# Kernel tuning notes

Measured on AMD Instinct MI355X. Metric: run time of the kernel, lower is better.

Reference implementation:

```python
import jax, jax.numpy as jnp
import numpy as np

N = 100000
IN_DIM = 256
HID = 64
HEADS = 2
OUT_DIM = 64
E = 1600000
NEG_SLOPE = 0.2


def gat_conv(x, edge_index, W, att_src, att_dst, bias):
    # PyG GATConv with heads=HEADS, concat=True, add_self_loops=True.
    # x: [N, IN_DIM]; edge_index: [2, E] (row0=src, row1=dst)
    loops = jnp.arange(N, dtype=edge_index.dtype)
    src = jnp.concatenate([edge_index[0], loops])  # [E+N]
    dst = jnp.concatenate([edge_index[1], loops])  # [E+N]
    h = (x @ W).reshape(N, HEADS, HID)             # [N, H, C]
    a_src = jnp.einsum('nhc,hc->nh', h, att_src)   # [N, H]
    a_dst = jnp.einsum('nhc,hc->nh', h, att_dst)   # [N, H]
    e = jax.nn.leaky_relu(a_src[src] + a_dst[dst], NEG_SLOPE)  # [E+N, H]
    # segment softmax over incoming edges of each dst node
    m = jax.ops.segment_max(e, dst, num_segments=N)            # [N, H]
    p = jnp.exp(e - m[dst])
    denom = jax.ops.segment_sum(p, dst, num_segments=N)        # [N, H]
    alpha = p / denom[dst]                                     # [E+N, H]
    msg = h[src] * alpha[:, :, None]                           # [E+N, H, C]
    out = jax.ops.segment_sum(msg, dst, num_segments=N)        # [N, H, C]
    return out.reshape(N, HEADS * HID) + bias


def setup_inputs() -> dict:
    key = jax.random.key(0)
    ks = jax.random.split(key, 12)
    s_in = 1.0 / np.sqrt(IN_DIM)
    s_h = 1.0 / np.sqrt(HID)
    s_fc = 1.0 / np.sqrt(HEADS * HID * 2)
    return {
        'x': jax.random.normal(ks[0], (N, IN_DIM), jnp.float32),
        'edge_index_connected': jax.random.randint(ks[1], (2, E), 0, N, jnp.int32),
        'edge_index_liked': jax.random.randint(ks[2], (2, E), 0, N, jnp.int32),
        'W1': jax.random.normal(ks[3], (IN_DIM, HEADS * HID), jnp.float32) * s_in,
        'att_src1': jax.random.normal(ks[4], (HEADS, HID), jnp.float32) * s_h,
        'att_dst1': jax.random.normal(ks[5], (HEADS, HID), jnp.float32) * s_h,
        'b1': jnp.zeros((HEADS * HID,), jnp.float32),
        'W2': jax.random.normal(ks[6], (IN_DIM, HEADS * HID), jnp.float32) * s_in,
        'att_src2': jax.random.normal(ks[7], (HEADS, HID), jnp.float32) * s_h,
        'att_dst2': jax.random.normal(ks[8], (HEADS, HID), jnp.float32) * s_h,
        'b2': jnp.zeros((HEADS * HID,), jnp.float32),
        'fc_W': jax.random.normal(ks[9], (HEADS * HID * 2, OUT_DIM), jnp.float32) * s_fc,
        'fc_b': jnp.zeros((OUT_DIM,), jnp.float32),
    }


def reference(x, edge_index_connected, edge_index_liked, W1, att_src1, att_dst1, b1,
              W2, att_src2, att_dst2, b2, fc_W, fc_b):
    xc = jax.nn.relu(gat_conv(x, edge_index_connected, W1, att_src1, att_dst1, b1))
    xl = jax.nn.relu(gat_conv(x, edge_index_liked, W2, att_src2, att_dst2, b2))
    x_comb = jnp.concatenate([xc, xl], axis=1)  # [N, 4*HID]
    return x_comb @ fc_W + fc_b
```

## Files before the change

### kernel.cpp

```cpp
#include <hip/hip_runtime.h>
#include <hip/hip_fp16.h>
#include <math.h>

#define NN 100000
#define IN_DIM 256
#define HCH 128
#define OUT_DIM 64
#define EE 1600000
#define NEG_SLOPE 0.2f

#define NB 1024
#define NPB 98
#define CAP 2048

typedef _Float16 half8v __attribute__((ext_vector_type(8)));
typedef _Float16 half4v __attribute__((ext_vector_type(4)));
typedef _Float16 half2v __attribute__((ext_vector_type(2)));
typedef __fp16 fp16x2 __attribute__((ext_vector_type(2)));
typedef float float4v __attribute__((ext_vector_type(4)));
typedef unsigned int u32;

union H2U { u32 u; fp16x2 h; };

__device__ __forceinline__ float lrelu(float v) { return v > 0.f ? v : NEG_SLOPE * v; }

__global__ void convw_kernel(const float* __restrict__ W0, const float* __restrict__ W1,
                             const float* __restrict__ fcW,
                             _Float16* __restrict__ wt, _Float16* __restrict__ fcw2)
{
    int i = blockIdx.x * 256 + threadIdx.x;
    if (i < 2 * IN_DIM * HCH) {
        int l = i >> 15, rem = i & 32767;
        int c = rem >> 8, k = rem & 255;
        const float* W = l ? W1 : W0;
        wt[i] = (_Float16)W[(size_t)k * HCH + c];
        return;
    }
    int j = i - 2 * IN_DIM * HCH;
    if (j < 256 * OUT_DIM) {
        int c = j >> 8, k = j & 255;
        fcw2[j] = (_Float16)fcW[(size_t)k * OUT_DIM + c];
    }
}

__global__ __launch_bounds__(256, 3) void gemm_mfma(
    const float* __restrict__ x, const _Float16* __restrict__ wt,
    const float* __restrict__ attS0, const float* __restrict__ attD0,
    const float* __restrict__ attS1, const float* __restrict__ attD1,
    _Float16* __restrict__ h16, float* __restrict__ a_s, float* __restrict__ a_d, int n)
{
    __shared__ _Float16 smem[64 * 72 + 256 * 72];
    __shared__ float attv[4][128];
    _Float16 (*As)[72] = (_Float16(*)[72])smem;
    _Float16 (*Bs)[72] = (_Float16(*)[72])(smem + 64 * 72);
    const int tid = threadIdx.x;
    const int lane = tid & 63, wave = tid >> 6;
    const int wm = wave & 1, wn = wave >> 1;
    const int q = lane >> 4, r16 = lane & 15;
    const int row0 = blockIdx.x * 64;

    if (tid < 128) {
        attv[0][tid] = attS0[tid]; attv[1][tid] = attD0[tid];
        attv[2][tid] = attS1[tid]; attv[3][tid] = attD1[tid];
    }

    float4v acc[2][8];
#pragma unroll
    for (int i = 0; i < 2; ++i)
#pragma unroll
        for (int j = 0; j < 8; ++j) acc[i][j] = (float4v){0.f, 0.f, 0.f, 0.f};

    const int ar = tid >> 2, aq = tid & 3;
    const bool rok = (row0 + ar) < n;
    for (int kt = 0; kt < IN_DIM; kt += 64) {
        const float* xp = x + (size_t)(row0 + ar) * IN_DIM + kt + aq * 16;
#pragma unroll
        for (int i = 0; i < 4; ++i) {
            float4 v = rok ? *(const float4*)(xp + i * 4) : make_float4(0.f, 0.f, 0.f, 0.f);
            half4v hv = { (_Float16)v.x, (_Float16)v.y, (_Float16)v.z, (_Float16)v.w };
            *(half4v*)&As[ar][aq * 16 + i * 4] = hv;
        }
        const _Float16* wp = wt + (size_t)tid * IN_DIM + kt;
#pragma unroll
        for (int i = 0; i < 8; ++i)
            *(half8v*)&Bs[tid][i * 8] = *(const half8v*)(wp + i * 8);
        __syncthreads();
#pragma unroll
        for (int s = 0; s < 2; ++s) {
            half8v af[2], bf[8];
#pragma unroll
            for (int t = 0; t < 2; ++t)
                af[t] = *(half8v*)&As[wm * 32 + t * 16 + r16][s * 32 + q * 8];
#pragma unroll
            for (int t = 0; t < 8; ++t)
                bf[t] = *(half8v*)&Bs[wn * 128 + t * 16 + r16][s * 32 + q * 8];
#pragma unroll
            for (int mt = 0; mt < 2; ++mt)
#pragma unroll
                for (int nt = 0; nt < 8; ++nt)
                    acc[mt][nt] = __builtin_amdgcn_mfma_f32_16x16x32_f16(
                        af[mt], bf[nt], acc[mt][nt], 0, 0, 0);
        }
        __syncthreads();
    }
    _Float16 (*eb)[264] = (_Float16(*)[264])smem;
#pragma unroll
    for (int mt = 0; mt < 2; ++mt) {
        const int er = wm * 32 + mt * 16 + q * 4;
#pragma unroll
        for (int reg = 0; reg < 4; ++reg)
#pragma unroll
            for (int nt = 0; nt < 8; ++nt)
                eb[er + reg][wn * 128 + nt * 16 + r16] = (_Float16)acc[mt][nt][reg];
    }
    __syncthreads();
    const int r = tid >> 2, qq = tid & 3;
    const int grow = row0 + r;
    if (grow < n) {
        const int l2 = qq >> 1;
        const int hh = qq & 1;
        const float* avS = &attv[l2 * 2 + 0][hh * 64];
        const float* avD = &attv[l2 * 2 + 1][hh * 64];
        _Float16* hout = h16 + (size_t)l2 * NN * HCH + (size_t)grow * HCH + hh * 64;
        float ds = 0.f, dd = 0.f;
#pragma unroll
        for (int i = 0; i < 8; ++i) {
            half8v v = *(half8v*)&eb[r][qq * 64 + i * 8];
            *(half8v*)(hout + i * 8) = v;
#pragma unroll
            for (int j = 0; j < 8; ++j) {
                float f = (float)v[j];
                ds = fmaf(f, avS[i * 8 + j], ds);
                dd = fmaf(f, avD[i * 8 + j], dd);
            }
        }
        a_s[(size_t)l2 * 2 * NN + 2 * grow + hh] = ds;
        a_d[(size_t)l2 * 2 * NN + 2 * grow + hh] = dd;
    }
}

__global__ __launch_bounds__(1024) void bucket_kernel(const int* __restrict__ ei0,
                                                      const int* __restrict__ ei1,
                                                      int* __restrict__ gcursor,
                                                      int* __restrict__ bstore, int e)
{
    __shared__ int hist[NB];
    __shared__ int base[NB];
    const int lay = blockIdx.y;
    const int* src = lay ? ei1 : ei0;
    const int* dst = src + e;
    int* gcur = gcursor + lay * NB;
    int* bst = bstore + (size_t)lay * NB * CAP;

    const int tid = threadIdx.x;
    const int per = (e + gridDim.x - 1) / gridDim.x;
    const int e0 = blockIdx.x * per;
    const int e1 = min(e, e0 + per);
    for (int i = tid; i < NB; i += 1024) hist[i] = 0;
    __syncthreads();
    for (int i = e0 + tid; i < e1; i += 1024)
        atomicAdd(&hist[dst[i] / NPB], 1);
    __syncthreads();
    for (int b = tid; b < NB; b += 1024) {
        int c = hist[b];
        base[b] = c ? atomicAdd(&gcur[b], c) : 0;
        hist[b] = 0;
    }
    __syncthreads();
    for (int i = e0 + tid; i < e1; i += 1024) {
        int d = dst[i];
        int s = src[i];
        int b = d / NPB;
        int pos = base[b] + atomicAdd(&hist[b], 1);
        if (pos >= 0 && pos < CAP) bst[b * CAP + pos] = (s << 7) | (d - b * NPB);
    }
}

__global__ __launch_bounds__(256) void sort_kernel(
    const int* __restrict__ gcursor, int* __restrict__ bstore,
    int* __restrict__ gstart, int* __restrict__ gend, int n)
{
    __shared__ int raw[CAP];
    __shared__ int sorted[CAP];
    __shared__ int curs[128];
    __shared__ int scanbuf[128];
    const int lay = blockIdx.y;
    const int* gcur = gcursor + lay * NB;
    int* bst = bstore + (size_t)lay * NB * CAP;
    int* gs = gstart + (size_t)lay * NN;
    int* ge = gend + (size_t)lay * NN;

    const int tid = threadIdx.x;
    const int b = blockIdx.x;
    const int node0 = b * NPB;
    const int nnode = min(NPB, n - node0);
    if (nnode <= 0) return;
    int cnt = gcur[b];
    cnt = cnt < 0 ? 0 : (cnt > CAP ? CAP : cnt);

    for (int i = tid; i < cnt; i += 256) raw[i] = bst[b * CAP + i];
    if (tid < 128) curs[tid] = 0;
    __syncthreads();
    for (int i = tid; i < cnt; i += 256) atomicAdd(&curs[raw[i] & 127], 1);
    __syncthreads();
    if (tid < 128) scanbuf[tid] = curs[tid];
    __syncthreads();
    for (int off = 1; off < 128; off <<= 1) {
        int v = 0;
        if (tid < 128) { v = scanbuf[tid]; if (tid >= off) v += scanbuf[tid - off]; }
        __syncthreads();
        if (tid < 128) scanbuf[tid] = v;
        __syncthreads();
    }
    if (tid < 128) {
        int ex = tid ? scanbuf[tid - 1] : 0;
        curs[tid] = ex;
        if (tid < nnode) {
            gs[node0 + tid] = b * CAP + ex;
            ge[node0 + tid] = b * CAP + scanbuf[tid];
        }
    }
    __syncthreads();
    for (int i = tid; i < cnt; i += 256) {
        int item = raw[i];
        int pos = atomicAdd(&curs[item & 127], 1);
        if (pos >= 0 && pos < CAP) sorted[pos] = item >> 7;
    }
    __syncthreads();
    for (int i = tid; i < cnt; i += 256) bst[b * CAP + i] = sorted[i];
}

__global__ __launch_bounds__(256) void agg_kernel(
    const _Float16* __restrict__ h16, const float2* __restrict__ a_s,
    const float2* __restrict__ a_d, const int* __restrict__ gstart,
    const int* __restrict__ gend, const int* __restrict__ bstore,
    const float* __restrict__ bias0, const float* __restrict__ bias1,
    _Float16* __restrict__ xc16, int n)
{
    __shared__ __align__(16) uint2 sh[4][64];
    const int lay = blockIdx.y;
    const _Float16* hL = h16 + (size_t)lay * NN * HCH;
    const float2* asL = a_s + (size_t)lay * NN;
    const float2* adL = a_d + (size_t)lay * NN;
    const int* gsL = gstart + (size_t)lay * NN;
    const int* geL = gend + (size_t)lay * NN;
    const int* ssort = bstore + (size_t)lay * NB * CAP;
    const float* bias = lay ? bias1 : bias0;

    const int wid = threadIdx.x >> 6, lane = threadIdx.x & 63;
    const int wbase = (blockIdx.x * 4 + wid) * 4;
    const int cl = lane & 15;
    const int w2 = lane >> 4;
    const int hh = cl >> 3;
    const u32 psel = hh ? 0x07060302u : 0x05040100u;
    const fp16x2 one2 = { (__fp16)1.f, (__fp16)1.f };

    float bv[8];
#pragma unroll
    for (int j = 0; j < 8; ++j) bv[j] = bias[cl * 8 + j];

    for (int ni = 0; ni < 4; ++ni) {
        const int node = wbase + ni;
        const bool valid = node < n;
        const int nn = valid ? node : 0;
        int start = gsL[nn], end = geL[nn];
        start = start < 0 ? 0 : (start > NB * CAP ? NB * CAP : start);
        end = end < start ? start : (end > NB * CAP ? NB * CAP : end);
        const float2 ad = adL[nn];
        const float2 asn = asL[nn];

        float acc[8] = {0.f, 0.f, 0.f, 0.f, 0.f, 0.f, 0.f, 0.f};
        float den = 0.f;

        for (int base = start; base < end; base += 64) {
            const int j = base + lane;
            const int cnt = min(64, end - base);
            float p0 = 0.f, p1 = 0.f;
            int s = 0;
            if (j < end) {
                s = ssort[j];
                if ((unsigned)s >= (unsigned)n) s = 0;
                float2 a = asL[s];
                p0 = __expf(lrelu(a.x + ad.x));
                p1 = __expf(lrelu(a.y + ad.y));
            }
            H2U pk; pk.h = __builtin_amdgcn_cvt_pkrtz(p0, p1);
            sh[wid][lane] = make_uint2((u32)s, pk.u);
            __builtin_amdgcn_wave_barrier();
            const int cnt8 = (cnt + 7) & ~7;
            for (int t = 0; t < cnt8; t += 8) {
                const uint4 rec = *(const uint4*)&sh[wid][t + 2 * w2];
                H2U pph; pph.u = __builtin_amdgcn_perm(rec.w, rec.y, psel);
                const half8v hv0 = *(const half8v*)(hL + ((rec.x << 7) | (u32)(cl << 3)));
                const half8v hv1 = *(const half8v*)(hL + ((rec.z << 7) | (u32)(cl << 3)));
                const u32* ap = (const u32*)&hv0;
                const u32* bp = (const u32*)&hv1;
#pragma unroll
                for (int d2 = 0; d2 < 4; ++d2) {
                    H2U pe, po;
                    pe.u = __builtin_amdgcn_perm(bp[d2], ap[d2], 0x05040100u);
                    po.u = __builtin_amdgcn_perm(bp[d2], ap[d2], 0x07060302u);
                    acc[2 * d2]     = __builtin_amdgcn_fdot2(pe.h, pph.h, acc[2 * d2], false);
                    acc[2 * d2 + 1] = __builtin_amdgcn_fdot2(po.h, pph.h, acc[2 * d2 + 1], false);
                }
                den = __builtin_amdgcn_fdot2(pph.h, one2, den, false);
            }
            __builtin_amdgcn_wave_barrier();
        }
        const float ps0 = __expf(lrelu(asn.x + ad.x));
        const float ps1 = __expf(lrelu(asn.y + ad.y));
        if (w2 == 0) {
            const half8v hv = *(const half8v*)(hL + (((u32)nn << 7) | (u32)(cl << 3)));
            const float pl = hh ? ps1 : ps0;
#pragma unroll
            for (int j2 = 0; j2 < 8; ++j2)
                acc[j2] = fmaf(pl, (float)hv[j2], acc[j2]);
            den += pl;
        }
#pragma unroll
        for (int j2 = 0; j2 < 8; ++j2) {
            acc[j2] += __shfl_xor(acc[j2], 16, 64);
            acc[j2] += __shfl_xor(acc[j2], 32, 64);
        }
        den += __shfl_xor(den, 16, 64);
        den += __shfl_xor(den, 32, 64);
        if (valid && lane < 16) {
            const float inv = 1.f / den;
            half8v o;
#pragma unroll
            for (int j2 = 0; j2 < 8; ++j2)
                o[j2] = (_Float16)fmaxf(acc[j2] * inv + bv[j2], 0.f);
            *(half8v*)(xc16 + (size_t)node * 256 + lay * HCH + cl * 8) = o;
        }
    }
}

__global__ __launch_bounds__(256) void fc_mfma(const _Float16* __restrict__ xc16,
                                               const _Float16* __restrict__ fw2,
                                               const float* __restrict__ fcb,
                                               float* __restrict__ out, int n)
{
    __shared__ _Float16 axs[64][264];
    const int tid = threadIdx.x;
    const int lane = tid & 63, wave = tid >> 6;
    const int q = lane >> 4, r16 = lane & 15;
    const int row0 = blockIdx.x * 64;

#pragma unroll
    for (int i = 0; i < 8; ++i) {
        const int idx = i * 256 + tid;
        const int row = idx >> 5;
        const int kg = (idx & 31) * 8;
        half8v v = { 0, 0, 0, 0, 0, 0, 0, 0 };
        if (row0 + row < n)
            v = *(const half8v*)(xc16 + (size_t)(row0 + row) * 256 + kg);
        *(half8v*)&axs[row][kg] = v;
    }
    __syncthreads();

    float4v acc[4];
#pragma unroll
    for (int i = 0; i < 4; ++i) acc[i] = (float4v){0.f, 0.f, 0.f, 0.f};
#pragma unroll
    for (int s = 0; s < 8; ++s) {
        const half8v af = *(half8v*)&axs[wave * 16 + r16][s * 32 + q * 8];
#pragma unroll
        for (int nt = 0; nt < 4; ++nt) {
            const half8v bf =
                *(const half8v*)(fw2 + (size_t)(nt * 16 + r16) * 256 + s * 32 + q * 8);
            acc[nt] = __builtin_amdgcn_mfma_f32_16x16x32_f16(af, bf, acc[nt], 0, 0, 0);
        }
    }
#pragma unroll
    for (int nt = 0; nt < 4; ++nt) {
        const int col = nt * 16 + r16;
#pragma unroll
        for (int reg = 0; reg < 4; ++reg) {
            const int row = row0 + wave * 16 + q * 4 + reg;
            if (row < n)
                out[(size_t)row * OUT_DIM + col] = acc[nt][reg] + fcb[col];
        }
    }
}

extern "C" void kernel_launch(void* const* d_in, const int* in_sizes, int n_in,
                              void* d_out, int out_size, void* d_ws, size_t ws_size,
                              hipStream_t stream)
{
    const float* x = (const float*)d_in[0];
    const int* ei[2] = { (const int*)d_in[1], (const int*)d_in[2] };
    const float* W[2] = { (const float*)d_in[3], (const float*)d_in[7] };
    const float* attS[2] = { (const float*)d_in[4], (const float*)d_in[8] };
    const float* attD[2] = { (const float*)d_in[5], (const float*)d_in[9] };
    const float* bias[2] = { (const float*)d_in[6], (const float*)d_in[10] };
    const float* fcW = (const float*)d_in[11];
    const float* fcb = (const float*)d_in[12];
    float* out = (float*)d_out;

    char* p = (char*)d_ws;
    size_t need = 0;
    auto carve = [&](size_t bytes) {
        char* r = p;
        size_t b = (bytes + 255) & ~(size_t)255;
        p += b;
        need += b;
        return r;
    };
    _Float16* h16 = (_Float16*)carve((size_t)2 * NN * HCH * 2);
    _Float16* xc16 = (_Float16*)carve((size_t)NN * 256 * 2);
    _Float16* wt = (_Float16*)carve((size_t)2 * IN_DIM * HCH * 2);
    _Float16* fcw2 = (_Float16*)carve((size_t)256 * OUT_DIM * 2);
    float* a_s = (float*)carve((size_t)2 * NN * 8);
    float* a_d = (float*)carve((size_t)2 * NN * 8);
    int* gcursor = (int*)carve((size_t)2 * NB * 4);
    int* bstore = (int*)carve((size_t)2 * NB * CAP * 4);
    int* gstart = (int*)carve((size_t)2 * NN * 4);
    int* gend = (int*)carve((size_t)2 * NN * 4);
    if (need > ws_size) return;

    const int gemm_blocks = (NN + 63) / 64;
    const int agg_blocks = (NN + 15) / 16;
    const int conv_total = 2 * IN_DIM * HCH + 256 * OUT_DIM;

    convw_kernel<<<(conv_total + 255) / 256, 256, 0, stream>>>(W[0], W[1], fcW, wt, fcw2);

    gemm_mfma<<<gemm_blocks, 256, 0, stream>>>(x, wt, attS[0], attD[0], attS[1], attD[1],
                                               h16, a_s, a_d, NN);

    (void)hipMemsetAsync(gcursor, 0, (size_t)2 * NB * 4, stream);
    bucket_kernel<<<dim3(256, 2), 1024, 0, stream>>>(ei[0], ei[1], gcursor, bstore, EE);
    sort_kernel<<<dim3(NB, 2), 256, 0, stream>>>(gcursor, bstore, gstart, gend, NN);
    agg_kernel<<<dim3(agg_blocks, 2), 256, 0, stream>>>(
        h16, (const float2*)a_s, (const float2*)a_d,
        gstart, gend, bstore, bias[0], bias[1], xc16, NN);
    fc_mfma<<<gemm_blocks, 256, 0, stream>>>(xc16, fcw2, fcb, out, NN);
}
```

Before: 464.9 us.

## Merge launches: fuse weight conversion with bucketing, GEMM with sort, aggregation with FC

The six launches become three. Weight conversion and edge bucketing share one grid, and the dense GEMM and per-bucket counting sort are interleaved across one grid. Aggregation of both layers now runs in a single block per 16 nodes, with the FC MFMA applied straight from shared memory. This removes the xc16 intermediate write and read plus the launch gaps, but it means smaller bucket blocks (256 threads) and possibly lower occupancy from the larger shared footprint in the fused kernels.

Result: slower. 478.7 us (+3.0%).

```diff
diff --git a/kernel.cpp b/kernel.cpp
--- a/kernel.cpp
+++ b/kernel.cpp
@@ -13,9 +13,13 @@
 #define NPB 98
 #define CAP 2048
 
+#define GEMM_BLOCKS 1563
+#define CONV_BLOCKS 320
+#define BUCKET_PER_LAYER 512
+#define SORT_BLOCKS (2 * NB)
+
 typedef _Float16 half8v __attribute__((ext_vector_type(8)));
 typedef _Float16 half4v __attribute__((ext_vector_type(4)));
-typedef _Float16 half2v __attribute__((ext_vector_type(2)));
 typedef __fp16 fp16x2 __attribute__((ext_vector_type(2)));
 typedef float float4v __attribute__((ext_vector_type(4)));
 typedef unsigned int u32;
@@ -24,40 +28,142 @@
 
 __device__ __forceinline__ float lrelu(float v) { return v > 0.f ? v : NEG_SLOPE * v; }
 
-__global__ void convw_kernel(const float* __restrict__ W0, const float* __restrict__ W1,
-                             const float* __restrict__ fcW,
-                             _Float16* __restrict__ wt, _Float16* __restrict__ fcw2)
+__global__ __launch_bounds__(256, 8) void prep_kernel(
+    const float* __restrict__ W0, const float* __restrict__ W1,
+    const float* __restrict__ fcW,
+    _Float16* __restrict__ wt, _Float16* __restrict__ fcw2,
+    const int* __restrict__ ei0, const int* __restrict__ ei1,
+    int* __restrict__ gcursor, int* __restrict__ bstore)
 {
-    int i = blockIdx.x * 256 + threadIdx.x;
-    if (i < 2 * IN_DIM * HCH) {
-        int l = i >> 15, rem = i & 32767;
-        int c = rem >> 8, k = rem & 255;
-        const float* W = l ? W1 : W0;
-        wt[i] = (_Float16)W[(size_t)k * HCH + c];
+    __shared__ int hist[NB];
+    __shared__ int base[NB];
+    const int tid = threadIdx.x;
+
+    if (blockIdx.x < CONV_BLOCKS) {
+        int i = blockIdx.x * 256 + tid;
+        if (i < 2 * IN_DIM * HCH) {
+            int l = i >> 15, rem = i & 32767;
+            int c = rem >> 8, k = rem & 255;
+            const float* W = l ? W1 : W0;
+            wt[i] = (_Float16)W[(size_t)k * HCH + c];
+            return;
+        }
+        int j = i - 2 * IN_DIM * HCH;
+        if (j < 256 * OUT_DIM) {
+            int c = j >> 8, k = j & 255;
+            fcw2[j] = (_Float16)fcW[(size_t)k * OUT_DIM + c];
+        }
         return;
     }
-    int j = i - 2 * IN_DIM * HCH;
-    if (j < 256 * OUT_DIM) {
-        int c = j >> 8, k = j & 255;
-        fcw2[j] = (_Float16)fcW[(size_t)k * OUT_DIM + c];
+
+    const int bb = blockIdx.x - CONV_BLOCKS;
+    const int lay = bb >> 9;
+    const int idx = bb & 511;
+    const int* src = lay ? ei1 : ei0;
+    const int* dst = src + EE;
+    int* gcur = gcursor + lay * NB;
+    int* bst = bstore + (size_t)lay * NB * CAP;
+
+    const int per = (EE + BUCKET_PER_LAYER - 1) / BUCKET_PER_LAYER;
+    const int e0 = idx * per;
+    const int e1 = min(EE, e0 + per);
+    for (int i = tid; i < NB; i += 256) hist[i] = 0;
+    __syncthreads();
+    for (int i = e0 + tid; i < e1; i += 256)
+        atomicAdd(&hist[dst[i] / NPB], 1);
+    __syncthreads();
+    for (int b = tid; b < NB; b += 256) {
+        int c = hist[b];
+        base[b] = c ? atomicAdd(&gcur[b], c) : 0;
+        hist[b] = 0;
+    }
+    __syncthreads();
+    for (int i = e0 + tid; i < e1; i += 256) {
+        int d = dst[i];
+        int s = src[i];
+        int b = d / NPB;
+        int pos = base[b] + atomicAdd(&hist[b], 1);
+        if (pos >= 0 && pos < CAP) bst[b * CAP + pos] = (s << 7) | (d - b * NPB);
     }
 }
 
-__global__ __launch_bounds__(256, 3) void gemm_mfma(
+__global__ __launch_bounds__(256, 3) void mid_kernel(
     const float* __restrict__ x, const _Float16* __restrict__ wt,
     const float* __restrict__ attS0, const float* __restrict__ attD0,
     const float* __restrict__ attS1, const float* __restrict__ attD1,
-    _Float16* __restrict__ h16, float* __restrict__ a_s, float* __restrict__ a_d, int n)
+    _Float16* __restrict__ h16, float* __restrict__ a_s, float* __restrict__ a_d,
+    const int* __restrict__ gcursor, int* __restrict__ bstore,
+    int* __restrict__ gstart, int* __restrict__ gend, int n)
 {
-    __shared__ _Float16 smem[64 * 72 + 256 * 72];
+    __shared__ __align__(16) _Float16 smem[64 * 72 + 256 * 72];
     __shared__ float attv[4][128];
+    const int tid = threadIdx.x;
+
+    const long long TS = SORT_BLOCKS;
+    const long long TB = GEMM_BLOCKS + SORT_BLOCKS;
+    const int k = blockIdx.x;
+    const int slo = (int)(((long long)k * TS) / TB);
+    const int shi = (int)(((long long)(k + 1) * TS) / TB);
+
+    if (shi > slo) {
+        int* raw = (int*)smem;
+        int* sorted = raw + CAP;
+        int* curs = sorted + CAP;
+        int* scanbuf = curs + 128;
+        const int sb = slo;
+        const int lay = sb >> 10;
+        const int b = sb & (NB - 1);
+        const int* gcur = gcursor + lay * NB;
+        int* bst = bstore + (size_t)lay * NB * CAP;
+        int* gs = gstart + (size_t)lay * NN;
+        int* ge = gend + (size_t)lay * NN;
+
+        const int node0 = b * NPB;
+        const int nnode = min(NPB, n - node0);
+        if (nnode <= 0) return;
+        int cnt = gcur[b];
+        cnt = cnt < 0 ? 0 : (cnt > CAP ? CAP : cnt);
+
+        for (int i = tid; i < cnt; i += 256) raw[i] = bst[b * CAP + i];
+        if (tid < 128) curs[tid] = 0;
+        __syncthreads();
+        for (int i = tid; i < cnt; i += 256) atomicAdd(&curs[raw[i] & 127], 1);
+        __syncthreads();
+        if (tid < 128) scanbuf[tid] = curs[tid];
+        __syncthreads();
+        for (int off = 1; off < 128; off <<= 1) {
+            int v = 0;
+            if (tid < 128) { v = scanbuf[tid]; if (tid >= off) v += scanbuf[tid - off]; }
+            __syncthreads();
+            if (tid < 128) scanbuf[tid] = v;
+            __syncthreads();
+        }
+        if (tid < 128) {
+            int ex = tid ? scanbuf[tid - 1] : 0;
+            curs[tid] = ex;
+            if (tid < nnode) {
+                gs[node0 + tid] = b * CAP + ex;
+                ge[node0 + tid] = b * CAP + scanbuf[tid];
+            }
+        }
+        __syncthreads();
+        for (int i = tid; i < cnt; i += 256) {
+            int item = raw[i];
+            int pos = atomicAdd(&curs[item & 127], 1);
+            if (pos >= 0 && pos < CAP) sorted[pos] = item >> 7;
+        }
+        __syncthreads();
+        for (int i = tid; i < cnt; i += 256) bst[b * CAP + i] = sorted[i];
+        return;
+    }
+
     _Float16 (*As)[72] = (_Float16(*)[72])smem;
     _Float16 (*Bs)[72] = (_Float16(*)[72])(smem + 64 * 72);
-    const int tid = threadIdx.x;
+    const int gb = k - slo;
     const int lane = tid & 63, wave = tid >> 6;
     const int wm = wave & 1, wn = wave >> 1;
     const int q = lane >> 4, r16 = lane & 15;
-    const int row0 = blockIdx.x * 64;
+    const int row0 = gb * 64;
 
     if (tid < 128) {
         attv[0][tid] = attS0[tid]; attv[1][tid] = attD0[tid];
@@ -139,247 +245,132 @@
     }
 }
 
-__global__ __launch_bounds__(1024) void bucket_kernel(const int* __restrict__ ei0,
-                                                      const int* __restrict__ ei1,
-                                                      int* __restrict__ gcursor,
-                                                      int* __restrict__ bstore, int e)
-{
-    __shared__ int hist[NB];
-    __shared__ int base[NB];
-    const int lay = blockIdx.y;
-    const int* src = lay ? ei1 : ei0;
-    const int* dst = src + e;
-    int* gcur = gcursor + lay * NB;
-    int* bst = bstore + (size_t)lay * NB * CAP;
-
-    const int tid = threadIdx.x;
-    const int per = (e + gridDim.x - 1) / gridDim.x;
-    const int e0 = blockIdx.x * per;
-    const int e1 = min(e, e0 + per);
-    for (int i = tid; i < NB; i += 1024) hist[i] = 0;
-    __syncthreads();
-    for (int i = e0 + tid; i < e1; i += 1024)
-        atomicAdd(&hist[dst[i] / NPB], 1);
-    __syncthreads();
-    for (int b = tid; b < NB; b += 1024) {
-        int c = hist[b];
-        base[b] = c ? atomicAdd(&gcur[b], c) : 0;
-        hist[b] = 0;
-    }
-    __syncthreads();
-    for (int i = e0 + tid; i < e1; i += 1024) {
-        int d = dst[i];
-        int s = src[i];
-        int b = d / NPB;
-        int pos = base[b] + atomicAdd(&hist[b], 1);
-        if (pos >= 0 && pos < CAP) bst[b * CAP + pos] = (s << 7) | (d - b * NPB);
-    }
-}
-
-__global__ __launch_bounds__(256) void sort_kernel(
-    const int* __restrict__ gcursor, int* __restrict__ bstore,
-    int* __restrict__ gstart, int* __restrict__ gend, int n)
-{
-    __shared__ int raw[CAP];
-    __shared__ int sorted[CAP];
-    __shared__ int curs[128];
-    __shared__ int scanbuf[128];
-    const int lay = blockIdx.y;
-    const int* gcur = gcursor + lay * NB;
-    int* bst = bstore + (size_t)lay * NB * CAP;
-    int* gs = gstart + (size_t)lay * NN;
-    int* ge = gend + (size_t)lay * NN;
-
-    const int tid = threadIdx.x;
-    const int b = blockIdx.x;
-    const int node0 = b * NPB;
-    const int nnode = min(NPB, n - node0);
-    if (nnode <= 0) return;
-    int cnt = gcur[b];
-    cnt = cnt < 0 ? 0 : (cnt > CAP ? CAP : cnt);
-
-    for (int i = tid; i < cnt; i += 256) raw[i] = bst[b * CAP + i];
-    if (tid < 128) curs[tid] = 0;
-    __syncthreads();
-    for (int i = tid; i < cnt; i += 256) atomicAdd(&curs[raw[i] & 127], 1);
-    __syncthreads();
-    if (tid < 128) scanbuf[tid] = curs[tid];
-    __syncthreads();
-    for (int off = 1; off < 128; off <<= 1) {
-        int v = 0;
-        if (tid < 128) { v = scanbuf[tid]; if (tid >= off) v += scanbuf[tid - off]; }
-        __syncthreads();
-        if (tid < 128) scanbuf[tid] = v;
-        __syncthreads();
-    }
-    if (tid < 128) {
-        int ex = tid ? scanbuf[tid - 1] : 0;
-        curs[tid] = ex;
-        if (tid < nnode) {
-            gs[node0 + tid] = b * CAP + ex;
-            ge[node0 + tid] = b * CAP + scanbuf[tid];
-        }
-    }
-    __syncthreads();
-    for (int i = tid; i < cnt; i += 256) {
-        int item = raw[i];
-        int pos = atomicAdd(&curs[item & 127], 1);
-        if (pos >= 0 && pos < CAP) sorted[pos] = item >> 7;
-    }
-    __syncthreads();
-    for (int i = tid; i < cnt; i += 256) bst[b * CAP + i] = sorted[i];
-}
-
-__global__ __launch_bounds__(256) void agg_kernel(
+__global__ __launch_bounds__(256) void agg_fc(
     const _Float16* __restrict__ h16, const float2* __restrict__ a_s,
     const float2* __restrict__ a_d, const int* __restrict__ gstart,
     const int* __restrict__ gend, const int* __restrict__ bstore,
     const float* __restrict__ bias0, const float* __restrict__ bias1,
-    _Float16* __restrict__ xc16, int n)
+    const _Float16* __restrict__ fw2, const float* __restrict__ fcb,
+    float* __restrict__ out, int n)
 {
     __shared__ __align__(16) uint2 sh[4][64];
-    const int lay = blockIdx.y;
-    const _Float16* hL = h16 + (size_t)lay * NN * HCH;
-    const float2* asL = a_s + (size_t)lay * NN;
-    const float2* adL = a_d + (size_t)lay * NN;
-    const int* gsL = gstart + (size_t)lay * NN;
-    const int* geL = gend + (size_t)lay * NN;
-    const int* ssort = bstore + (size_t)lay * NB * CAP;
-    const float* bias = lay ? bias1 : bias0;
-
-    const int wid = threadIdx.x >> 6, lane = threadIdx.x & 63;
-    const int wbase = (blockIdx.x * 4 + wid) * 4;
+    __shared__ __align__(16) _Float16 xcs[16][264];
+    const int tid = threadIdx.x;
+    const int wid = tid >> 6, lane = tid & 63;
+    const int wbase = blockIdx.x * 16 + wid * 4;
     const int cl = lane & 15;
     const int w2 = lane >> 4;
     const int hh = cl >> 3;
     const u32 psel = hh ? 0x07060302u : 0x05040100u;
     const fp16x2 one2 = { (__fp16)1.f, (__fp16)1.f };
 
-    float bv[8];
-#pragma unroll
-    for (int j = 0; j < 8; ++j) bv[j] = bias[cl * 8 + j];
+    float bv[2][8];
+#pragma unroll
+    for (int j = 0; j < 8; ++j) {
+        bv[0][j] = bias0[cl * 8 + j];
+        bv[1][j] = bias1[cl * 8 + j];
+    }
 
     for (int ni = 0; ni < 4; ++ni) {
         const int node = wbase + ni;
         const bool valid = node < n;
         const int nn = valid ? node : 0;
-        int start = gsL[nn], end = geL[nn];
-        start = start < 0 ? 0 : (start > NB * CAP ? NB * CAP : start);
-        end = end < start ? start : (end > NB * CAP ? NB * CAP : end);
-        const float2 ad = adL[nn];
-        const float2 asn = asL[nn];
-
-        float acc[8] = {0.f, 0.f, 0.f, 0.f, 0.f, 0.f, 0.f, 0.f};
-        float den = 0.f;
-
-        for (int base = start; base < end; base += 64) {
-            const int j = base + lane;
-            const int cnt = min(64, end - base);
-            float p0 = 0.f, p1 = 0.f;
-            int s = 0;
-            if (j < end) {
-                s = ssort[j];
-                if ((unsigned)s >= (unsigned)n) s = 0;
-                float2 a = asL[s];
-                p0 = __expf(lrelu(a.x + ad.x));
-                p1 = __expf(lrelu(a.y + ad.y));
-            }
-            H2U pk; pk.h = __builtin_amdgcn_cvt_pkrtz(p0, p1);
-            sh[wid][lane] = make_uint2((u32)s, pk.u);
-            __builtin_amdgcn_wave_barrier();
-            const int cnt8 = (cnt + 7) & ~7;
-            for (int t = 0; t < cnt8; t += 8) {
-                const uint4 rec = *(const uint4*)&sh[wid][t + 2 * w2];
-                H2U pph; pph.u = __builtin_amdgcn_perm(rec.w, rec.y, psel);
-                const half8v hv0 = *(const half8v*)(hL + ((rec.x << 7) | (u32)(cl << 3)));
-                const half8v hv1 = *(const half8v*)(hL + ((rec.z << 7) | (u32)(cl << 3)));
-                const u32* ap = (const u32*)&hv0;
-                const u32* bp = (const u32*)&hv1;
-#pragma unroll
-                for (int d2 = 0; d2 < 4; ++d2) {
-                    H2U pe, po;
-                    pe.u = __builtin_amdgcn_perm(bp[d2], ap[d2], 0x05040100u);
-                    po.u = __builtin_amdgcn_perm(bp[d2], ap[d2], 0x07060302u);
-                    acc[2 * d2]     = __builtin_amdgcn_fdot2(pe.h, pph.h, acc[2 * d2], false);
-                    acc[2 * d2 + 1] = __builtin_amdgcn_fdot2(po.h, pph.h, acc[2 * d2 + 1], false);
+        const int xr = wid * 4 + ni;
+        for (int lay = 0; lay < 2; ++lay) {
+            const _Float16* hL = h16 + (size_t)lay * NN * HCH;
+            const float2* asL = a_s + (size_t)lay * NN;
+            const float2* adL = a_d + (size_t)lay * NN;
+            const int* ssort = bstore + (size_t)lay * NB * CAP;
+            int start = gstart[(size_t)lay * NN + nn];
+            int end = gend[(size_t)lay * NN + nn];
+            start = start < 0 ? 0 : (start > NB * CAP ? NB * CAP : start);
+            end = end < start ? start : (end > NB * CAP ? NB * CAP : end);
+            const float2 ad = adL[nn];
+            const float2 asn = asL[nn];
+
+            float acc[8] = {0.f, 0.f, 0.f, 0.f, 0.f, 0.f, 0.f, 0.f};
+            float den = 0.f;
+
+            for (int base2 = start; base2 < end; base2 += 64) {
+                const int j = base2 + lane;
+                const int cnt = min(64, end - base2);
+                float p0 = 0.f, p1 = 0.f;
+                int s = 0;
+                if (j < end) {
+                    s = ssort[j];
+                    if ((unsigned)s >= (unsigned)n) s = 0;
+                    float2 a = asL[s];
+                    p0 = __expf(lrelu(a.x + ad.x));
+                    p1 = __expf(lrelu(a.y + ad.y));
                 }
-                den = __builtin_amdgcn_fdot2(pph.h, one2, den, false);
-            }
-            __builtin_amdgcn_wave_barrier();
-        }
-        const float ps0 = __expf(lrelu(asn.x + ad.x));
-        const float ps1 = __expf(lrelu(asn.y + ad.y));
-        if (w2 == 0) {
-            const half8v hv = *(const half8v*)(hL + (((u32)nn << 7) | (u32)(cl << 3)));
-            const float pl = hh ? ps1 : ps0;
-#pragma unroll
-            for (int j2 = 0; j2 < 8; ++j2)
-                acc[j2] = fmaf(pl, (float)hv[j2], acc[j2]);
-            den += pl;
-        }
-#pragma unroll
-        for (int j2 = 0; j2 < 8; ++j2) {
-            acc[j2] += __shfl_xor(acc[j2], 16, 64);
-            acc[j2] += __shfl_xor(acc[j2], 32, 64);
-        }
-        den += __shfl_xor(den, 16, 64);
-        den += __shfl_xor(den, 32, 64);
-        if (valid && lane < 16) {
-            const float inv = 1.f / den;
-            half8v o;
-#pragma unroll
-            for (int j2 = 0; j2 < 8; ++j2)
-                o[j2] = (_Float16)fmaxf(acc[j2] * inv + bv[j2], 0.f);
-            *(half8v*)(xc16 + (size_t)node * 256 + lay * HCH + cl * 8) = o;
-        }
-    }
-}
-
-__global__ __launch_bounds__(256) void fc_mfma(const _Float16* __restrict__ xc16,
-                                               const _Float16* __restrict__ fw2,
-                                               const float* __restrict__ fcb,
-                                               float* __restrict__ out, int n)
-{
-    __shared__ _Float16 axs[64][264];
-    const int tid = threadIdx.x;
-    const int lane = tid & 63, wave = tid >> 6;
+                H2U pk; pk.h = __builtin_amdgcn_cvt_pkrtz(p0, p1);
+                sh[wid][lane] = make_uint2((u32)s, pk.u);
+                __builtin_amdgcn_wave_barrier();
+                const int cnt8 = (cnt + 7) & ~7;
+                for (int t = 0; t < cnt8; t += 8) {
+                    const uint4 rec = *(const uint4*)&sh[wid][t + 2 * w2];
+                    H2U pph; pph.u = __builtin_amdgcn_perm(rec.w, rec.y, psel);
+                    const half8v hv0 = *(const half8v*)(hL + ((rec.x << 7) | (u32)(cl << 3)));
+                    const half8v hv1 = *(const half8v*)(hL + ((rec.z << 7) | (u32)(cl << 3)));
+                    const u32* ap = (const u32*)&hv0;
+                    const u32* bp = (const u32*)&hv1;
+#pragma unroll
+                    for (int d2 = 0; d2 < 4; ++d2) {
+                        H2U pe, po;
+                        pe.u = __builtin_amdgcn_perm(bp[d2], ap[d2], 0x05040100u);
+                        po.u = __builtin_amdgcn_perm(bp[d2], ap[d2], 0x07060302u);
+                        acc[2 * d2]     = __builtin_amdgcn_fdot2(pe.h, pph.h, acc[2 * d2], false);
+                        acc[2 * d2 + 1] = __builtin_amdgcn_fdot2(po.h, pph.h, acc[2 * d2 + 1], false);
+                    }
+                    den = __builtin_amdgcn_fdot2(pph.h, one2, den, false);
+                }
+                __builtin_amdgcn_wave_barrier();
+            }
+            const float ps0 = __expf(lrelu(asn.x + ad.x));
+            const float ps1 = __expf(lrelu(asn.y + ad.y));
+            if (w2 == 0) {
+                const half8v hv = *(const half8v*)(hL + (((u32)nn << 7) | (u32)(cl << 3)));
+                const float pl = hh ? ps1 : ps0;
+#pragma unroll
+                for (int j2 = 0; j2 < 8; ++j2)
+                    acc[j2] = fmaf(pl, (float)hv[j2], acc[j2]);
+                den += pl;
+            }
+#pragma unroll
+            for (int j2 = 0; j2 < 8; ++j2) {
+                acc[j2] += __shfl_xor(acc[j2], 16, 64);
+                acc[j2] += __shfl_xor(acc[j2], 32, 64);
+            }
+            den += __shfl_xor(den, 16, 64);
+            den += __shfl_xor(den, 32, 64);
+            if (lane < 16) {
+                const float inv = 1.f / den;
+                half8v o;
+#pragma unroll
+                for (int j2 = 0; j2 < 8; ++j2)
+                    o[j2] = (_Float16)fmaxf(acc[j2] * inv + bv[lay][j2], 0.f);
+                *(half8v*)&xcs[xr][lay * HCH + cl * 8] = o;
+            }
+        }
+    }
+    __syncthreads();
+
     const int q = lane >> 4, r16 = lane & 15;
-    const int row0 = blockIdx.x * 64;
-
-#pragma unroll
-    for (int i = 0; i < 8; ++i) {
-        const int idx = i * 256 + tid;
-        const int row = idx >> 5;
-        const int kg = (idx & 31) * 8;
-        half8v v = { 0, 0, 0, 0, 0, 0, 0, 0 };
-        if (row0 + row < n)
-            v = *(const half8v*)(xc16 + (size_t)(row0 + row) * 256 + kg);
-        *(half8v*)&axs[row][kg] = v;
-    }
-    __syncthreads();
-
-    float4v acc[4];
-#pragma unroll
-    for (int i = 0; i < 4; ++i) acc[i] = (float4v){0.f, 0.f, 0.f, 0.f};
+    float4v facc = (float4v){0.f, 0.f, 0.f, 0.f};
 #pragma unroll
     for (int s = 0; s < 8; ++s) {
-        const half8v af = *(half8v*)&axs[wave * 16 + r16][s * 32 + q * 8];
-#pragma unroll
-        for (int nt = 0; nt < 4; ++nt) {
-            const half8v bf =
-                *(const half8v*)(fw2 + (size_t)(nt * 16 + r16) * 256 + s * 32 + q * 8);
-            acc[nt] = __builtin_amdgcn_mfma_f32_16x16x32_f16(af, bf, acc[nt], 0, 0, 0);
-        }
-    }
-#pragma unroll
-    for (int nt = 0; nt < 4; ++nt) {
-        const int col = nt * 16 + r16;
-#pragma unroll
-        for (int reg = 0; reg < 4; ++reg) {
-            const int row = row0 + wave * 16 + q * 4 + reg;
-            if (row < n)
-                out[(size_t)row * OUT_DIM + col] = acc[nt][reg] + fcb[col];
-        }
+        const half8v af = *(half8v*)&xcs[r16][s * 32 + q * 8];
+        const half8v bf =
+            *(const half8v*)(fw2 + (size_t)(wid * 16 + r16) * 256 + s * 32 + q * 8);
+        facc = __builtin_amdgcn_mfma_f32_16x16x32_f16(af, bf, facc, 0, 0, 0);
+    }
+    const int col = wid * 16 + r16;
+    const float fb = fcb[col];
+#pragma unroll
+    for (int reg = 0; reg < 4; ++reg) {
+        const int grow = blockIdx.x * 16 + q * 4 + reg;
+        if (grow < n)
+            out[(size_t)grow * OUT_DIM + col] = facc[reg] + fb;
     }
 }
 
@@ -407,7 +398,6 @@
         return r;
     };
     _Float16* h16 = (_Float16*)carve((size_t)2 * NN * HCH * 2);
-    _Float16* xc16 = (_Float16*)carve((size_t)NN * 256 * 2);
     _Float16* wt = (_Float16*)carve((size_t)2 * IN_DIM * HCH * 2);
     _Float16* fcw2 = (_Float16*)carve((size_t)256 * OUT_DIM * 2);
     float* a_s = (float*)carve((size_t)2 * NN * 8);
@@ -418,20 +408,16 @@
     int* gend = (int*)carve((size_t)2 * NN * 4);
     if (need > ws_size) return;
 
-    const int gemm_blocks = (NN + 63) / 64;
-    const int agg_blocks = (NN + 15) / 16;
-    const int conv_total = 2 * IN_DIM * HCH + 256 * OUT_DIM;
-
-    convw_kernel<<<(conv_total + 255) / 256, 256, 0, stream>>>(W[0], W[1], fcW, wt, fcw2);
-
-    gemm_mfma<<<gemm_blocks, 256, 0, stream>>>(x, wt, attS[0], attD[0], attS[1], attD[1],
-                                               h16, a_s, a_d, NN);
-
     (void)hipMemsetAsync(gcursor, 0, (size_t)2 * NB * 4, stream);
-    bucket_kernel<<<dim3(256, 2), 1024, 0, stream>>>(ei[0], ei[1], gcursor, bstore, EE);
-    sort_kernel<<<dim3(NB, 2), 256, 0, stream>>>(gcursor, bstore, gstart, gend, NN);
-    agg_kernel<<<dim3(agg_blocks, 2), 256, 0, stream>>>(
+
+    prep_kernel<<<CONV_BLOCKS + 2 * BUCKET_PER_LAYER, 256, 0, stream>>>(
+        W[0], W[1], fcW, wt, fcw2, ei[0], ei[1], gcursor, bstore);
+
+    mid_kernel<<<GEMM_BLOCKS + SORT_BLOCKS, 256, 0, stream>>>(
+        x, wt, attS[0], attD[0], attS[1], attD[1],
+        h16, a_s, a_d, gcursor, bstore, gstart, gend, NN);
+
+    agg_fc<<<(NN + 15) / 16, 256, 0, stream>>>(
         h16, (const float2*)a_s, (const float2*)a_d,
-        gstart, gend, bstore, bias[0], bias[1], xc16, NN);
-    fc_mfma<<<gemm_blocks, 256, 0, stream>>>(xc16, fcw2, fcb, out, NN);
+        gstart, gend, bstore, bias[0], bias[1], fcw2, fcb, out, NN);
 }
```
